# Optimization experiments

Hardware: AMD Instinct MI355X
Metric: run time of the kernel (lower is better)

Reference implementation:

```python
import jax, jax.numpy as jnp
import numpy as np

B, N_N, N_A, D = 1024, 96, 96, 512


def _normalize(x):
    return x / jnp.linalg.norm(x, axis=-1, keepdims=True)


def setup_inputs() -> dict:
    key = jax.random.key(0)
    ks = jax.random.split(key, 8)
    img_embs = _normalize(jax.random.normal(ks[0], (B, D), jnp.float32))
    normal_text_embs = _normalize(jax.random.normal(ks[1], (N_N, D), jnp.float32))
    abnormal_text_embs = _normalize(jax.random.normal(ks[2], (N_A, D), jnp.float32))
    logit_scale = jnp.full((1,), np.log(100.0), jnp.float32)  # CLIP temperature
    W1 = jax.random.normal(ks[3], (2 * D, D), jnp.float32) / np.sqrt(2 * D)
    b1 = jnp.zeros((D,), jnp.float32)
    W2 = jax.random.normal(ks[4], (D, D // 2), jnp.float32) / np.sqrt(D)
    b2 = jnp.zeros((D // 2,), jnp.float32)
    W3 = jax.random.normal(ks[5], (D // 2, D // 4), jnp.float32) / np.sqrt(D // 2)
    b3 = jnp.zeros((D // 4,), jnp.float32)
    return {"img_embs": img_embs, "normal_text_embs": normal_text_embs,
            "abnormal_text_embs": abnormal_text_embs, "logit_scale": logit_scale,
            "W1": W1, "b1": b1, "W2": W2, "b2": b2, "W3": W3, "b3": b3}


def _mlp(x, W1, b1, W2, b2, W3, b3):
    h = jax.nn.relu(x @ W1 + b1)
    h = jax.nn.relu(h @ W2 + b2)
    return h @ W3 + b3


def _branch(img_embs, text_embs, scale, W1, b1, W2, b2, W3, b3):
    # sims: [B, N]; softmax weights then exp-scaled text embeddings
    sims = (img_embs @ text_embs.T) * scale
    w = jax.nn.softmax(sims, axis=-1)
    scaled_text = text_embs[None, :, :] * jnp.exp(w)[:, :, None]      # [B, N, D]
    rep_img = jnp.broadcast_to(img_embs[:, None, :], scaled_text.shape)  # [B, N, D]
    x = jnp.concatenate([rep_img, scaled_text], axis=-1)              # [B, N, 2D]
    h = _mlp(x, W1, b1, W2, b2, W3, b3)                               # [B, N, D//4]
    return h.mean(axis=1)                                             # [B, D//4]


def reference(img_embs, normal_text_embs, abnormal_text_embs, logit_scale,
              W1, b1, W2, b2, W3, b3):
    scale = jnp.exp(logit_scale[0])
    h_n = _branch(img_embs, normal_text_embs, scale, W1, b1, W2, b2, W3, b3)
    h_a = _branch(img_embs, abnormal_text_embs, scale, W1, b1, W2, b2, W3, b3)
    return (h_n, h_a)
```

## Files before the change

kernel.cpp:

```cpp
#include <hip/hip_runtime.h>
#include <hip/hip_bf16.h>


typedef __attribute__((ext_vector_type(8))) short short8;
typedef __attribute__((ext_vector_type(4))) float floatx4;
typedef __attribute__((ext_vector_type(4))) unsigned int uint4v;

__device__ __forceinline__ unsigned short f2bf(float x) {
    unsigned int u = __float_as_uint(x);
    u += 0x7fffu + ((u >> 16) & 1u);
    return (unsigned short)(u >> 16);
}
__device__ __forceinline__ float bf2f(unsigned short u) {
    return __uint_as_float(((unsigned int)u) << 16);
}

template <bool BF16OUT>
__device__ __forceinline__ void gemm32(
    const float* __restrict__ A0, const float* __restrict__ A1, int rows0,
    const float* __restrict__ Bm, float* __restrict__ Cf,
    unsigned short* __restrict__ Cb, int mt, int nt, float* sAT, int t) {
    int r0 = mt * 32, c0 = nt * 64;
    int rg = t >> 4, cg = t & 15;
    int lrow = t >> 3, k4 = (t & 7) * 4;
    int gr = r0 + lrow;
    const float* Ap = (gr < rows0) ? (A0 + gr * 512) : (A1 + (gr - rows0) * 512);
    float acc[2][4];
#pragma unroll
    for (int r = 0; r < 2; r++)
#pragma unroll
        for (int c = 0; c < 4; c++) acc[r][c] = 0.f;
    const float* Bp = Bm + c0 + cg * 4;
    for (int k0 = 0; k0 < 512; k0 += 32) {
        __syncthreads();
        float4 av = *(const float4*)(Ap + k0 + k4);
        sAT[(k4 + 0) * 34 + lrow] = av.x;
        sAT[(k4 + 1) * 34 + lrow] = av.y;
        sAT[(k4 + 2) * 34 + lrow] = av.z;
        sAT[(k4 + 3) * 34 + lrow] = av.w;
        __syncthreads();
#pragma unroll 8
        for (int kk = 0; kk < 32; kk++) {
            float a0 = sAT[kk * 34 + rg * 2];
            float a1 = sAT[kk * 34 + rg * 2 + 1];
            float4 bv = *(const float4*)(Bp + (k0 + kk) * 512);
            acc[0][0] = fmaf(a0, bv.x, acc[0][0]); acc[0][1] = fmaf(a0, bv.y, acc[0][1]);
            acc[0][2] = fmaf(a0, bv.z, acc[0][2]); acc[0][3] = fmaf(a0, bv.w, acc[0][3]);
            acc[1][0] = fmaf(a1, bv.x, acc[1][0]); acc[1][1] = fmaf(a1, bv.y, acc[1][1]);
            acc[1][2] = fmaf(a1, bv.z, acc[1][2]); acc[1][3] = fmaf(a1, bv.w, acc[1][3]);
        }
    }
    int rr = r0 + rg * 2, cc = c0 + cg * 4;
#pragma unroll
    for (int r = 0; r < 2; r++) {
        if (BF16OUT) {
            unsigned long long pk =
                (unsigned long long)f2bf(acc[r][0]) | ((unsigned long long)f2bf(acc[r][1]) << 16) |
                ((unsigned long long)f2bf(acc[r][2]) << 32) | ((unsigned long long)f2bf(acc[r][3]) << 48);
            *(unsigned long long*)(Cb + (rr + r) * 512 + cc) = pk;
        } else {
            *(float4*)(Cf + (rr + r) * 512 + cc) = make_float4(acc[r][0], acc[r][1], acc[r][2], acc[r][3]);
        }
    }
}

__global__ __launch_bounds__(256) void prep_kernel(
    const float* __restrict__ img, const float* __restrict__ tn,
    const float* __restrict__ ta, const float* __restrict__ ls,
    const float* __restrict__ W1, const float* __restrict__ W2,
    float* __restrict__ e_ws, float* __restrict__ U_ws,
    unsigned short* __restrict__ Tb, unsigned short* __restrict__ W2Tf) {
    __shared__ __align__(16) float smem[8704];
    int idx = blockIdx.x;
    int t = threadIdx.x;

    if (idx < 256) {
        int bi0 = idx * 4;
        float* sImg = smem;
        float* sS   = smem + 2064;
        float* sMx  = smem + 2832;
        float* sSum = smem + 2840;
#pragma unroll
        for (int p = 0; p < 2; p++) {
            int i4 = t + 256 * p;
            int i = i4 >> 7, k4 = (i4 & 127) * 4;
            float4 v = *(const float4*)(img + (bi0 + i) * 512 + k4);
            sImg[i * 516 + k4 + 0] = v.x; sImg[i * 516 + k4 + 1] = v.y;
            sImg[i * 516 + k4 + 2] = v.z; sImg[i * 516 + k4 + 3] = v.w;
        }
        __syncthreads();
        float scale = __expf(ls[0]);
        int i = t & 3, n0 = (t >> 2) * 3;
        const float* txp[3];
#pragma unroll
        for (int r = 0; r < 3; r++) {
            int n = n0 + r;
            txp[r] = (n < 96) ? (tn + n * 512) : (ta + (n - 96) * 512);
        }
        float d0 = 0.f, d1 = 0.f, d2 = 0.f;
        const float* ib = &sImg[i * 516];
#pragma unroll 4
        for (int k4 = 0; k4 < 512; k4 += 4) {
            float4 iv = *(const float4*)(ib + k4);
            float4 a = *(const float4*)(txp[0] + k4);
            float4 b = *(const float4*)(txp[1] + k4);
            float4 c = *(const float4*)(txp[2] + k4);
            d0 += iv.x * a.x + iv.y * a.y + iv.z * a.z + iv.w * a.w;
            d1 += iv.x * b.x + iv.y * b.y + iv.z * b.z + iv.w * b.w;
            d2 += iv.x * c.x + iv.y * c.y + iv.z * c.z + iv.w * c.w;
        }
        sS[i * 192 + n0 + 0] = d0 * scale;
        sS[i * 192 + n0 + 1] = d1 * scale;
        sS[i * 192 + n0 + 2] = d2 * scale;
        __syncthreads();
        if (t < 8) {
            int ii = t >> 1, brx = t & 1;
            const float* base = &sS[ii * 192 + brx * 96];
            float m = -1e30f;
            for (int n = 0; n < 96; n++) m = fmaxf(m, base[n]);
            float s = 0.f;
            for (int n = 0; n < 96; n++) s += __expf(base[n] - m);
            sMx[t] = m; sSum[t] = s;
        }
        __syncthreads();
#pragma unroll
        for (int p = 0; p < 3; p++) {
            int j = t + 256 * p;
            int ii = j & 3, n = j >> 2;
            int brx = (n >= 96) ? 1 : 0;
            int nn = n - brx * 96;
            float w = __expf(sS[ii * 192 + n] - sMx[ii * 2 + brx]) / sSum[ii * 2 + brx];
            e_ws[(brx * 1024 + bi0 + ii) * 96 + nn] = __expf(w);
        }
    } else if (idx < 512) {
        int i2 = idx - 256;
        gemm32<false>(img, img, 1 << 20, W1, U_ws, nullptr, i2 >> 3, i2 & 7, smem, t);
    } else if (idx < 560) {
        int i2 = idx - 512;
        gemm32<true>(tn, ta, 96, W1 + 512 * 512, nullptr, Tb, i2 >> 3, i2 & 7, smem, t);
    } else {
        int kt = idx - 560;
        int k0 = kt * 32;
        float* sWT = smem;
        int kr = t >> 3, n0 = (t & 7) * 32;
#pragma unroll
        for (int c = 0; c < 8; c++) {
            float4 v = *(const float4*)(W2 + (k0 + kr) * 256 + n0 + c * 4);
            sWT[(n0 + c * 4 + 0) * 33 + kr] = v.x;
            sWT[(n0 + c * 4 + 1) * 33 + kr] = v.y;
            sWT[(n0 + c * 4 + 2) * 33 + kr] = v.z;
            sWT[(n0 + c * 4 + 3) * 33 + kr] = v.w;
        }
        __syncthreads();
        int lane = t & 63;
        int kl = (lane >> 4) * 8;
#pragma unroll
        for (int it = 0; it < 4; it++) {
            int nt = it * 4 + (t >> 6);
            int n = nt * 16 + (lane & 15);
            uint4v u;
#pragma unroll
            for (int c = 0; c < 4; c++) {
                unsigned short lo = f2bf(sWT[n * 33 + kl + 2 * c]);
                unsigned short hi = f2bf(sWT[n * 33 + kl + 2 * c + 1]);
                u[c] = (unsigned int)lo | ((unsigned int)hi << 16);
            }
            *(uint4v*)(W2Tf + (((kt * 16 + nt) * 64) + lane) * 8) = u;
        }
    }
}

__global__ __launch_bounds__(256, 4) void branch_mlp6(
    const float* __restrict__ U, const unsigned short* __restrict__ Tb,
    const float* __restrict__ e_all, const unsigned short* __restrict__ W2Tf,
    const float* __restrict__ b1, const float* __restrict__ b2,
    float* __restrict__ m2p) {
    int b = blockIdx.x, br = blockIdx.y, half = blockIdx.z;
    const unsigned short* T = Tb + br * (96 * 512) + half * (48 * 512);

    __shared__ float sUb[512];
    __shared__ float sE[48];
    __shared__ __align__(16) unsigned short sH[2][48 * 64];

    int t = threadIdx.x;
    sUb[t] = U[b * 512 + t] + b1[t];
    sUb[t + 256] = U[b * 512 + t + 256] + b1[t + 256];
    if (t < 48) sE[t] = e_all[(br * 1024 + b) * 96 + half * 48 + t];
    __syncthreads();

    const int wave = t >> 6, lane = t & 63;
    const int frow = lane & 15, fkq = (lane >> 4) * 8;
    const int f7 = frow & 7;
    const int srow = t >> 3;
    const int skc = (t & 7) * 8;
    const bool two = (t < 128);
    const int srow2 = 32 + (t >> 3);

    const floatx4 fz = {0.f, 0.f, 0.f, 0.f};
    floatx4 acc[3][4];
#pragma unroll
    for (int mt = 0; mt < 3; mt++)
#pragma unroll
        for (int j = 0; j < 4; j++) acc[mt][j] = fz;

    float ev0 = sE[srow];
    float ev1 = two ? sE[srow2] : 0.f;
    const int sw1 = skc ^ ((srow & 7) * 8);
    const int sw2 = skc ^ ((srow2 & 7) * 8);

    const unsigned short* Wf = W2Tf + (wave * 4 * 64 + lane) * 8;
    short8 bpre[4];
#pragma unroll
    for (int j = 0; j < 4; j++)
        bpre[j] = *(const short8*)(Wf + j * (64 * 8));

#pragma unroll
    for (int s = 0; s < 8; s++) {
        int k0 = s * 64;
        unsigned short* sHb = sH[s & 1];
        float4 u0 = *(const float4*)(&sUb[k0 + skc]);
        float4 u1 = *(const float4*)(&sUb[k0 + skc + 4]);
        float ua[8] = {u0.x, u0.y, u0.z, u0.w, u1.x, u1.y, u1.z, u1.w};
        short8 tv0 = *(const short8*)(T + srow * 512 + k0 + skc);
        {
            uint4v pk;
#pragma unroll
            for (int jj = 0; jj < 4; jj++) {
                float f0 = fmaxf(fmaf(ev0, bf2f((unsigned short)tv0[2 * jj]), ua[2 * jj]), 0.f);
                float f1 = fmaxf(fmaf(ev0, bf2f((unsigned short)tv0[2 * jj + 1]), ua[2 * jj + 1]), 0.f);
                __hip_bfloat162 h2 = __float22bfloat162_rn(make_float2(f0, f1));
                unsigned int bits; __builtin_memcpy(&bits, &h2, 4);
                pk[jj] = bits;
            }
            *(uint4v*)(&sHb[srow * 64 + sw1]) = pk;
        }
        if (two) {
            short8 tv1 = *(const short8*)(T + srow2 * 512 + k0 + skc);
            uint4v pk;
#pragma unroll
            for (int jj = 0; jj < 4; jj++) {
                float f0 = fmaxf(fmaf(ev1, bf2f((unsigned short)tv1[2 * jj]), ua[2 * jj]), 0.f);
                float f1 = fmaxf(fmaf(ev1, bf2f((unsigned short)tv1[2 * jj + 1]), ua[2 * jj + 1]), 0.f);
                __hip_bfloat162 h2 = __float22bfloat162_rn(make_float2(f0, f1));
                unsigned int bits; __builtin_memcpy(&bits, &h2, 4);
                pk[jj] = bits;
            }
            *(uint4v*)(&sHb[srow2 * 64 + sw2]) = pk;
        }
        __syncthreads();
        short8 b1f[4];
#pragma unroll
        for (int j = 0; j < 4; j++)
            b1f[j] = *(const short8*)(Wf + ((2 * s + 1) * 16 + j) * (64 * 8));
        const int ka0 = (((fkq >> 3) ^ f7) << 3);
        const int ka1 = (((4 + (fkq >> 3)) ^ f7) << 3);
#pragma unroll
        for (int mt = 0; mt < 3; mt++) {
            short8 afr = *(const short8*)(&sHb[(mt * 16 + frow) * 64 + ka0]);
#pragma unroll
            for (int j = 0; j < 4; j++)
                acc[mt][j] = __builtin_amdgcn_mfma_f32_16x16x32_bf16(afr, bpre[j], acc[mt][j], 0, 0, 0);
        }
        if (s < 7) {
#pragma unroll
            for (int j = 0; j < 4; j++)
                bpre[j] = *(const short8*)(Wf + ((2 * s + 2) * 16 + j) * (64 * 8));
        }
#pragma unroll
        for (int mt = 0; mt < 3; mt++) {
            short8 afr = *(const short8*)(&sHb[(mt * 16 + frow) * 64 + ka1]);
#pragma unroll
            for (int j = 0; j < 4; j++)
                acc[mt][j] = __builtin_amdgcn_mfma_f32_16x16x32_bf16(afr, b1f[j], acc[mt][j], 0, 0, 0);
        }
    }

#pragma unroll
    for (int j = 0; j < 4; j++) {
        int col = wave * 64 + j * 16 + frow;
        float bb = b2[col];
        float s = 0.f;
#pragma unroll
        for (int mt = 0; mt < 3; mt++)
#pragma unroll
            for (int r = 0; r < 4; r++)
                s += fmaxf(acc[mt][j][r] + bb, 0.f);
        s += __shfl_xor(s, 16);
        s += __shfl_xor(s, 32);
        if (lane < 16)
            m2p[(((half * 2 + br) * 1024) + b) * 256 + col] = s;
    }
}

__global__ __launch_bounds__(128) void out_kernel(
    const float* __restrict__ m2p, const float* __restrict__ W3,
    const float* __restrict__ b3, float* __restrict__ out) {
    int b = blockIdx.x, br = blockIdx.y;
    int t = threadIdx.x;
    __shared__ float sM[256];
    const float* p0 = m2p + ((0 + br) * 1024 + b) * 256;
    const float* p1 = m2p + ((2 + br) * 1024 + b) * 256;
    sM[t]       = (p0[t]       + p1[t])       * (1.0f / 96.0f);
    sM[t + 128] = (p0[t + 128] + p1[t + 128]) * (1.0f / 96.0f);
    __syncthreads();
    float o = b3[t];
#pragma unroll 8
    for (int k = 0; k < 256; k++) o = fmaf(sM[k], W3[k * 128 + t], o);
    out[(br * 1024 + b) * 128 + t] = o;
}

extern "C" void kernel_launch(void* const* d_in, const int* in_sizes, int n_in,
                              void* d_out, int out_size, void* d_ws, size_t ws_size,
                              hipStream_t stream) {
    const float* img = (const float*)d_in[0];
    const float* tn  = (const float*)d_in[1];
    const float* ta  = (const float*)d_in[2];
    const float* ls  = (const float*)d_in[3];
    const float* W1  = (const float*)d_in[4];
    const float* b1  = (const float*)d_in[5];
    const float* W2  = (const float*)d_in[6];
    const float* b2  = (const float*)d_in[7];
    const float* W3  = (const float*)d_in[8];
    const float* b3  = (const float*)d_in[9];
    float* out = (float*)d_out;
    float* ws  = (float*)d_ws;

    float* e_ws = ws;
    float* U_ws = ws + 196608;
    unsigned short* Tb   = (unsigned short*)(ws + 720896);
    unsigned short* W2Tf = (unsigned short*)(ws + 770048);
    float* m2p = ws + 835584;

    prep_kernel<<<576, 256, 0, stream>>>(img, tn, ta, ls, W1, W2, e_ws, U_ws, Tb, W2Tf);
    branch_mlp6<<<dim3(1024, 2, 2), 256, 0, stream>>>(U_ws, Tb, e_ws, W2Tf, b1, b2, m2p);
    out_kernel<<<dim3(1024, 2), 128, 0, stream>>>(m2p, W3, b3, out);
}
```

Measured before the change: 193.3 us.

## Software-pipeline H tile construction with MFMA in branch MLP kernel

Restructures the K loop so that the bf16 hidden tile for the next 64-wide K slice is built into the alternate shared buffer after the current slice's MFMAs, with the global loads for T and the W2 fragments issued before the MFMAs. A prologue builds the first tile and hoists the swizzle offsets, and the initial global loads are issued before the first barrier. The intent is to hide global-load latency and the elementwise work behind matrix-core work. It needs more registers for the prefetched fragments, which may lower occupancy under the 256x4 launch bound.

```diff
diff --git a/kernel.cpp b/kernel.cpp
--- a/kernel.cpp
+++ b/kernel.cpp
@@ -170,7 +170,7 @@
     }
 }
 
-__global__ __launch_bounds__(256, 4) void branch_mlp6(
+__global__ __launch_bounds__(256, 4) void branch_mlp7(
     const float* __restrict__ U, const unsigned short* __restrict__ Tb,
     const float* __restrict__ e_all, const unsigned short* __restrict__ W2Tf,
     const float* __restrict__ b1, const float* __restrict__ b2,
@@ -186,7 +186,6 @@
     sUb[t] = U[b * 512 + t] + b1[t];
     sUb[t + 256] = U[b * 512 + t + 256] + b1[t + 256];
     if (t < 48) sE[t] = e_all[(br * 1024 + b) * 96 + half * 48 + t];
-    __syncthreads();
 
     const int wave = t >> 6, lane = t & 63;
     const int frow = lane & 15, fkq = (lane >> 4) * 8;
@@ -195,6 +194,10 @@
     const int skc = (t & 7) * 8;
     const bool two = (t < 128);
     const int srow2 = 32 + (t >> 3);
+    const int sw1 = skc ^ ((srow & 7) * 8);
+    const int sw2 = skc ^ ((srow2 & 7) * 8);
+    const int ka0 = (((fkq >> 3) ^ f7) << 3);
+    const int ka1 = (((4 + (fkq >> 3)) ^ f7) << 3);
 
     const floatx4 fz = {0.f, 0.f, 0.f, 0.f};
     floatx4 acc[3][4];
@@ -203,26 +206,90 @@
 #pragma unroll
         for (int j = 0; j < 4; j++) acc[mt][j] = fz;
 
+    short8 tv0 = *(const short8*)(T + srow * 512 + skc);
+    short8 tv1 = two ? *(const short8*)(T + srow2 * 512 + skc) : tv0;
+    const unsigned short* Wf = W2Tf + (wave * 4 * 64 + lane) * 8;
+    short8 bpre[4];
+#pragma unroll
+    for (int j = 0; j < 4; j++)
+        bpre[j] = *(const short8*)(Wf + j * (64 * 8));
+
+    __syncthreads();
+
     float ev0 = sE[srow];
     float ev1 = two ? sE[srow2] : 0.f;
-    const int sw1 = skc ^ ((srow & 7) * 8);
-    const int sw2 = skc ^ ((srow2 & 7) * 8);
-
-    const unsigned short* Wf = W2Tf + (wave * 4 * 64 + lane) * 8;
-    short8 bpre[4];
-#pragma unroll
-    for (int j = 0; j < 4; j++)
-        bpre[j] = *(const short8*)(Wf + j * (64 * 8));
+
+    {
+        float4 u0 = *(const float4*)(&sUb[skc]);
+        float4 u1 = *(const float4*)(&sUb[skc + 4]);
+        float ua[8] = {u0.x, u0.y, u0.z, u0.w, u1.x, u1.y, u1.z, u1.w};
+        uint4v pk;
+#pragma unroll
+        for (int jj = 0; jj < 4; jj++) {
+            float f0 = fmaxf(fmaf(ev0, bf2f((unsigned short)tv0[2 * jj]), ua[2 * jj]), 0.f);
+            float f1 = fmaxf(fmaf(ev0, bf2f((unsigned short)tv0[2 * jj + 1]), ua[2 * jj + 1]), 0.f);
+            __hip_bfloat162 h2 = __float22bfloat162_rn(make_float2(f0, f1));
+            unsigned int bits; __builtin_memcpy(&bits, &h2, 4);
+            pk[jj] = bits;
+        }
+        *(uint4v*)(&sH[0][srow * 64 + sw1]) = pk;
+        if (two) {
+            uint4v pk2;
+#pragma unroll
+            for (int jj = 0; jj < 4; jj++) {
+                float f0 = fmaxf(fmaf(ev1, bf2f((unsigned short)tv1[2 * jj]), ua[2 * jj]), 0.f);
+                float f1 = fmaxf(fmaf(ev1, bf2f((unsigned short)tv1[2 * jj + 1]), ua[2 * jj + 1]), 0.f);
+                __hip_bfloat162 h2 = __float22bfloat162_rn(make_float2(f0, f1));
+                unsigned int bits; __builtin_memcpy(&bits, &h2, 4);
+                pk2[jj] = bits;
+            }
+            *(uint4v*)(&sH[0][srow2 * 64 + sw2]) = pk2;
+        }
+    }
 
 #pragma unroll
     for (int s = 0; s < 8; s++) {
         int k0 = s * 64;
         unsigned short* sHb = sH[s & 1];
-        float4 u0 = *(const float4*)(&sUb[k0 + skc]);
-        float4 u1 = *(const float4*)(&sUb[k0 + skc + 4]);
-        float ua[8] = {u0.x, u0.y, u0.z, u0.w, u1.x, u1.y, u1.z, u1.w};
-        short8 tv0 = *(const short8*)(T + srow * 512 + k0 + skc);
-        {
+        __syncthreads();
+
+        short8 b1f[4];
+#pragma unroll
+        for (int j = 0; j < 4; j++)
+            b1f[j] = *(const short8*)(Wf + ((2 * s + 1) * 16 + j) * (64 * 8));
+        if (s < 7) {
+            tv0 = *(const short8*)(T + srow * 512 + k0 + 64 + skc);
+            if (two) tv1 = *(const short8*)(T + srow2 * 512 + k0 + 64 + skc);
+        }
+        short8 bnext[4];
+        if (s < 7) {
+#pragma unroll
+            for (int j = 0; j < 4; j++)
+                bnext[j] = *(const short8*)(Wf + ((2 * s + 2) * 16 + j) * (64 * 8));
+        }
+
+#pragma unroll
+        for (int mt = 0; mt < 3; mt++) {
+            short8 afr = *(const short8*)(&sHb[(mt * 16 + frow) * 64 + ka0]);
+#pragma unroll
+            for (int j = 0; j < 4; j++)
+                acc[mt][j] = __builtin_amdgcn_mfma_f32_16x16x32_bf16(afr, bpre[j], acc[mt][j], 0, 0, 0);
+        }
+#pragma unroll
+        for (int mt = 0; mt < 3; mt++) {
+            short8 afr = *(const short8*)(&sHb[(mt * 16 + frow) * 64 + ka1]);
+#pragma unroll
+            for (int j = 0; j < 4; j++)
+                acc[mt][j] = __builtin_amdgcn_mfma_f32_16x16x32_bf16(afr, b1f[j], acc[mt][j], 0, 0, 0);
+        }
+#pragma unroll
+        for (int j = 0; j < 4; j++) bpre[j] = bnext[j];
+
+        if (s < 7) {
+            unsigned short* sHn = sH[(s + 1) & 1];
+            float4 u0 = *(const float4*)(&sUb[k0 + 64 + skc]);
+            float4 u1 = *(const float4*)(&sUb[k0 + 64 + skc + 4]);
+            float ua[8] = {u0.x, u0.y, u0.z, u0.w, u1.x, u1.y, u1.z, u1.w};
             uint4v pk;
 #pragma unroll
             for (int jj = 0; jj < 4; jj++) {
@@ -232,46 +299,19 @@
                 unsigned int bits; __builtin_memcpy(&bits, &h2, 4);
                 pk[jj] = bits;
             }
-            *(uint4v*)(&sHb[srow * 64 + sw1]) = pk;
-        }
-        if (two) {
-            short8 tv1 = *(const short8*)(T + srow2 * 512 + k0 + skc);
-            uint4v pk;
-#pragma unroll
-            for (int jj = 0; jj < 4; jj++) {
-                float f0 = fmaxf(fmaf(ev1, bf2f((unsigned short)tv1[2 * jj]), ua[2 * jj]), 0.f);
-                float f1 = fmaxf(fmaf(ev1, bf2f((unsigned short)tv1[2 * jj + 1]), ua[2 * jj + 1]), 0.f);
-                __hip_bfloat162 h2 = __float22bfloat162_rn(make_float2(f0, f1));
-                unsigned int bits; __builtin_memcpy(&bits, &h2, 4);
-                pk[jj] = bits;
+            *(uint4v*)(&sHn[srow * 64 + sw1]) = pk;
+            if (two) {
+                uint4v pk2;
+#pragma unroll
+                for (int jj = 0; jj < 4; jj++) {
+                    float f0 = fmaxf(fmaf(ev1, bf2f((unsigned short)tv1[2 * jj]), ua[2 * jj]), 0.f);
+                    float f1 = fmaxf(fmaf(ev1, bf2f((unsigned short)tv1[2 * jj + 1]), ua[2 * jj + 1]), 0.f);
+                    __hip_bfloat162 h2 = __float22bfloat162_rn(make_float2(f0, f1));
+                    unsigned int bits; __builtin_memcpy(&bits, &h2, 4);
+                    pk2[jj] = bits;
+                }
+                *(uint4v*)(&sHn[srow2 * 64 + sw2]) = pk2;
             }
-            *(uint4v*)(&sHb[srow2 * 64 + sw2]) = pk;
-        }
-        __syncthreads();
-        short8 b1f[4];
-#pragma unroll
-        for (int j = 0; j < 4; j++)
-            b1f[j] = *(const short8*)(Wf + ((2 * s + 1) * 16 + j) * (64 * 8));
-        const int ka0 = (((fkq >> 3) ^ f7) << 3);
-        const int ka1 = (((4 + (fkq >> 3)) ^ f7) << 3);
-#pragma unroll
-        for (int mt = 0; mt < 3; mt++) {
-            short8 afr = *(const short8*)(&sHb[(mt * 16 + frow) * 64 + ka0]);
-#pragma unroll
-            for (int j = 0; j < 4; j++)
-                acc[mt][j] = __builtin_amdgcn_mfma_f32_16x16x32_bf16(afr, bpre[j], acc[mt][j], 0, 0, 0);
-        }
-        if (s < 7) {
-#pragma unroll
-            for (int j = 0; j < 4; j++)
-                bpre[j] = *(const short8*)(Wf + ((2 * s + 2) * 16 + j) * (64 * 8));
-        }
-#pragma unroll
-        for (int mt = 0; mt < 3; mt++) {
-            short8 afr = *(const short8*)(&sHb[(mt * 16 + frow) * 64 + ka1]);
-#pragma unroll
-            for (int j = 0; j < 4; j++)
-                acc[mt][j] = __builtin_amdgcn_mfma_f32_16x16x32_bf16(afr, b1f[j], acc[mt][j], 0, 0, 0);
         }
     }
 
@@ -332,6 +372,6 @@
     float* m2p = ws + 835584;
 
     prep_kernel<<<576, 256, 0, stream>>>(img, tn, ta, ls, W1, W2, e_ws, U_ws, Tb, W2Tf);
-    branch_mlp6<<<dim3(1024, 2, 2), 256, 0, stream>>>(U_ws, Tb, e_ws, W2Tf, b1, b2, m2p);
+    branch_mlp7<<<dim3(1024, 2, 2), 256, 0, stream>>>(U_ws, Tb, e_ws, W2Tf, b1, b2, m2p);
     out_kernel<<<dim3(1024, 2), 128, 0, stream>>>(m2p, W3, b3, out);
 }
```

Result: faster. 187.2 us (-3.2%).

## Process all 96 rows per block, pipeline staging, and fuse W3 output projection

Applied to the files above, without the earlier changes.

Each block now handles all 96 text rows of one (batch, branch) pair instead of splitting across two halves. This doubles the MFMA accumulators per wave and reuses each W2 fragment load across twice as many rows. The next k-slice of T and W2 is loaded and staged into the other shared buffer while the current MFMAs run, leaving one barrier per step. The final W3 projection and mean are fused into the kernel, which removes the partial-sum workspace round trip and the separate launch. The cost is higher register pressure, with occupancy lowered to 3 blocks per SM, and half as many blocks.

```diff
diff --git a/kernel.cpp b/kernel.cpp
--- a/kernel.cpp
+++ b/kernel.cpp
@@ -4,6 +4,7 @@
 
 typedef __attribute__((ext_vector_type(8))) short short8;
 typedef __attribute__((ext_vector_type(4))) float floatx4;
+typedef __attribute__((ext_vector_type(2))) float float2v;
 typedef __attribute__((ext_vector_type(4))) unsigned int uint4v;
 
 __device__ __forceinline__ unsigned short f2bf(float x) {
@@ -170,108 +171,133 @@
     }
 }
 
-__global__ __launch_bounds__(256, 4) void branch_mlp6(
+__device__ __forceinline__ uint4v stage8(float ev, short8 tv, const float2v* u2) {
+    uint4v tp; __builtin_memcpy(&tp, &tv, 16);
+    float2v e2 = {ev, ev};
+    const float2v z2 = {0.f, 0.f};
+    uint4v pk;
+#pragma unroll
+    for (int jj = 0; jj < 4; jj++) {
+        float2v t2;
+        t2.x = __uint_as_float(tp[jj] << 16);
+        t2.y = __uint_as_float(tp[jj] & 0xffff0000u);
+        float2v f = __builtin_elementwise_fma(e2, t2, u2[jj]);
+        f = __builtin_elementwise_max(f, z2);
+        __hip_bfloat162 h2 = __float22bfloat162_rn(make_float2(f.x, f.y));
+        unsigned int bits; __builtin_memcpy(&bits, &h2, 4);
+        pk[jj] = bits;
+    }
+    return pk;
+}
+
+__global__ __launch_bounds__(256, 3) void branch_mlp8(
     const float* __restrict__ U, const unsigned short* __restrict__ Tb,
     const float* __restrict__ e_all, const unsigned short* __restrict__ W2Tf,
     const float* __restrict__ b1, const float* __restrict__ b2,
-    float* __restrict__ m2p) {
-    int b = blockIdx.x, br = blockIdx.y, half = blockIdx.z;
-    const unsigned short* T = Tb + br * (96 * 512) + half * (48 * 512);
+    const float* __restrict__ W3, const float* __restrict__ b3,
+    float* __restrict__ out) {
+    int b = blockIdx.x, br = blockIdx.y;
+    const unsigned short* T = Tb + br * (96 * 512);
 
     __shared__ float sUb[512];
-    __shared__ float sE[48];
-    __shared__ __align__(16) unsigned short sH[2][48 * 64];
+    __shared__ float sE[96];
+    __shared__ __align__(16) unsigned short sH[2][96 * 64];
+    __shared__ float sM2[256];
+    __shared__ float sPart[256];
 
     int t = threadIdx.x;
     sUb[t] = U[b * 512 + t] + b1[t];
     sUb[t + 256] = U[b * 512 + t + 256] + b1[t + 256];
-    if (t < 48) sE[t] = e_all[(br * 1024 + b) * 96 + half * 48 + t];
-    __syncthreads();
+    if (t < 96) sE[t] = e_all[(br * 1024 + b) * 96 + t];
 
     const int wave = t >> 6, lane = t & 63;
     const int frow = lane & 15, fkq = (lane >> 4) * 8;
     const int f7 = frow & 7;
     const int srow = t >> 3;
     const int skc = (t & 7) * 8;
-    const bool two = (t < 128);
-    const int srow2 = 32 + (t >> 3);
+    const int sw = skc ^ ((srow & 7) * 8);
+    const int ka0 = (((fkq >> 3) ^ f7) << 3);
+    const int ka1 = (((4 + (fkq >> 3)) ^ f7) << 3);
 
     const floatx4 fz = {0.f, 0.f, 0.f, 0.f};
-    floatx4 acc[3][4];
-#pragma unroll
-    for (int mt = 0; mt < 3; mt++)
+    floatx4 acc[6][4];
+#pragma unroll
+    for (int mt = 0; mt < 6; mt++)
 #pragma unroll
         for (int j = 0; j < 4; j++) acc[mt][j] = fz;
 
-    float ev0 = sE[srow];
-    float ev1 = two ? sE[srow2] : 0.f;
-    const int sw1 = skc ^ ((srow & 7) * 8);
-    const int sw2 = skc ^ ((srow2 & 7) * 8);
-
+    short8 tv[3];
+#pragma unroll
+    for (int i2 = 0; i2 < 3; i2++)
+        tv[i2] = *(const short8*)(T + (srow + 32 * i2) * 512 + skc);
     const unsigned short* Wf = W2Tf + (wave * 4 * 64 + lane) * 8;
     short8 bpre[4];
 #pragma unroll
     for (int j = 0; j < 4; j++)
         bpre[j] = *(const short8*)(Wf + j * (64 * 8));
+
+    __syncthreads();
+
+    float ev[3];
+#pragma unroll
+    for (int i2 = 0; i2 < 3; i2++) ev[i2] = sE[srow + 32 * i2];
+
+    {
+        float2v u2[4];
+#pragma unroll
+        for (int jj = 0; jj < 4; jj++) u2[jj] = *(const float2v*)(&sUb[skc + 2 * jj]);
+#pragma unroll
+        for (int i2 = 0; i2 < 3; i2++)
+            *(uint4v*)(&sH[0][(srow + 32 * i2) * 64 + sw]) = stage8(ev[i2], tv[i2], u2);
+    }
 
 #pragma unroll
     for (int s = 0; s < 8; s++) {
         int k0 = s * 64;
         unsigned short* sHb = sH[s & 1];
-        float4 u0 = *(const float4*)(&sUb[k0 + skc]);
-        float4 u1 = *(const float4*)(&sUb[k0 + skc + 4]);
-        float ua[8] = {u0.x, u0.y, u0.z, u0.w, u1.x, u1.y, u1.z, u1.w};
-        short8 tv0 = *(const short8*)(T + srow * 512 + k0 + skc);
-        {
-            uint4v pk;
-#pragma unroll
-            for (int jj = 0; jj < 4; jj++) {
-                float f0 = fmaxf(fmaf(ev0, bf2f((unsigned short)tv0[2 * jj]), ua[2 * jj]), 0.f);
-                float f1 = fmaxf(fmaf(ev0, bf2f((unsigned short)tv0[2 * jj + 1]), ua[2 * jj + 1]), 0.f);
-                __hip_bfloat162 h2 = __float22bfloat162_rn(make_float2(f0, f1));
-                unsigned int bits; __builtin_memcpy(&bits, &h2, 4);
-                pk[jj] = bits;
-            }
-            *(uint4v*)(&sHb[srow * 64 + sw1]) = pk;
-        }
-        if (two) {
-            short8 tv1 = *(const short8*)(T + srow2 * 512 + k0 + skc);
-            uint4v pk;
-#pragma unroll
-            for (int jj = 0; jj < 4; jj++) {
-                float f0 = fmaxf(fmaf(ev1, bf2f((unsigned short)tv1[2 * jj]), ua[2 * jj]), 0.f);
-                float f1 = fmaxf(fmaf(ev1, bf2f((unsigned short)tv1[2 * jj + 1]), ua[2 * jj + 1]), 0.f);
-                __hip_bfloat162 h2 = __float22bfloat162_rn(make_float2(f0, f1));
-                unsigned int bits; __builtin_memcpy(&bits, &h2, 4);
-                pk[jj] = bits;
-            }
-            *(uint4v*)(&sHb[srow2 * 64 + sw2]) = pk;
-        }
-        __syncthreads();
+        __syncthreads();
+
         short8 b1f[4];
 #pragma unroll
         for (int j = 0; j < 4; j++)
             b1f[j] = *(const short8*)(Wf + ((2 * s + 1) * 16 + j) * (64 * 8));
-        const int ka0 = (((fkq >> 3) ^ f7) << 3);
-        const int ka1 = (((4 + (fkq >> 3)) ^ f7) << 3);
-#pragma unroll
-        for (int mt = 0; mt < 3; mt++) {
+        if (s < 7) {
+#pragma unroll
+            for (int i2 = 0; i2 < 3; i2++)
+                tv[i2] = *(const short8*)(T + (srow + 32 * i2) * 512 + k0 + 64 + skc);
+        }
+        short8 bnext[4];
+        if (s < 7) {
+#pragma unroll
+            for (int j = 0; j < 4; j++)
+                bnext[j] = *(const short8*)(Wf + ((2 * s + 2) * 16 + j) * (64 * 8));
+        }
+
+#pragma unroll
+        for (int mt = 0; mt < 6; mt++) {
             short8 afr = *(const short8*)(&sHb[(mt * 16 + frow) * 64 + ka0]);
 #pragma unroll
             for (int j = 0; j < 4; j++)
                 acc[mt][j] = __builtin_amdgcn_mfma_f32_16x16x32_bf16(afr, bpre[j], acc[mt][j], 0, 0, 0);
         }
-        if (s < 7) {
-#pragma unroll
-            for (int j = 0; j < 4; j++)
-                bpre[j] = *(const short8*)(Wf + ((2 * s + 2) * 16 + j) * (64 * 8));
-        }
-#pragma unroll
-        for (int mt = 0; mt < 3; mt++) {
+#pragma unroll
+        for (int mt = 0; mt < 6; mt++) {
             short8 afr = *(const short8*)(&sHb[(mt * 16 + frow) * 64 + ka1]);
 #pragma unroll
             for (int j = 0; j < 4; j++)
                 acc[mt][j] = __builtin_amdgcn_mfma_f32_16x16x32_bf16(afr, b1f[j], acc[mt][j], 0, 0, 0);
+        }
+#pragma unroll
+        for (int j = 0; j < 4; j++) bpre[j] = bnext[j];
+
+        if (s < 7) {
+            unsigned short* sHn = sH[(s + 1) & 1];
+            float2v u2[4];
+#pragma unroll
+            for (int jj = 0; jj < 4; jj++) u2[jj] = *(const float2v*)(&sUb[k0 + 64 + skc + 2 * jj]);
+#pragma unroll
+            for (int i2 = 0; i2 < 3; i2++)
+                *(uint4v*)(&sHn[(srow + 32 * i2) * 64 + sw]) = stage8(ev[i2], tv[i2], u2);
         }
     }
 
@@ -281,32 +307,25 @@
         float bb = b2[col];
         float s = 0.f;
 #pragma unroll
-        for (int mt = 0; mt < 3; mt++)
+        for (int mt = 0; mt < 6; mt++)
 #pragma unroll
             for (int r = 0; r < 4; r++)
                 s += fmaxf(acc[mt][j][r] + bb, 0.f);
         s += __shfl_xor(s, 16);
         s += __shfl_xor(s, 32);
-        if (lane < 16)
-            m2p[(((half * 2 + br) * 1024) + b) * 256 + col] = s;
-    }
-}
-
-__global__ __launch_bounds__(128) void out_kernel(
-    const float* __restrict__ m2p, const float* __restrict__ W3,
-    const float* __restrict__ b3, float* __restrict__ out) {
-    int b = blockIdx.x, br = blockIdx.y;
-    int t = threadIdx.x;
-    __shared__ float sM[256];
-    const float* p0 = m2p + ((0 + br) * 1024 + b) * 256;
-    const float* p1 = m2p + ((2 + br) * 1024 + b) * 256;
-    sM[t]       = (p0[t]       + p1[t])       * (1.0f / 96.0f);
-    sM[t + 128] = (p0[t + 128] + p1[t + 128]) * (1.0f / 96.0f);
+        if (lane < 16) sM2[col] = s * (1.0f / 96.0f);
+    }
     __syncthreads();
-    float o = b3[t];
+
+    int col = t & 127, ks2 = t >> 7;
+    const float* w3p = W3 + (ks2 * 128) * 128 + col;
+    const float* mp = sM2 + ks2 * 128;
+    float o = 0.f;
 #pragma unroll 8
-    for (int k = 0; k < 256; k++) o = fmaf(sM[k], W3[k * 128 + t], o);
-    out[(br * 1024 + b) * 128 + t] = o;
+    for (int k = 0; k < 128; k++) o = fmaf(mp[k], w3p[k * 128], o);
+    sPart[t] = o;
+    __syncthreads();
+    if (t < 128) out[(br * 1024 + b) * 128 + t] = sPart[t] + sPart[t + 128] + b3[t];
 }
 
 extern "C" void kernel_launch(void* const* d_in, const int* in_sizes, int n_in,
@@ -329,9 +348,7 @@
     float* U_ws = ws + 196608;
     unsigned short* Tb   = (unsigned short*)(ws + 720896);
     unsigned short* W2Tf = (unsigned short*)(ws + 770048);
-    float* m2p = ws + 835584;
 
     prep_kernel<<<576, 256, 0, stream>>>(img, tn, ta, ls, W1, W2, e_ws, U_ws, Tb, W2Tf);
-    branch_mlp6<<<dim3(1024, 2, 2), 256, 0, stream>>>(U_ws, Tb, e_ws, W2Tf, b1, b2, m2p);
-    out_kernel<<<dim3(1024, 2), 128, 0, stream>>>(m2p, W3, b3, out);
-}
+    branch_mlp8<<<dim3(1024, 2), 256, 0, stream>>>(U_ws, Tb, e_ws, W2Tf, b1, b2, W3, b3, out);
+}
```

New measurement: 176.5 us. 1.09x faster.
